# Kernel tuning notes

Measured on AMD Instinct MI355X. Metric: run time of the kernel, lower is better.

The kernel has to match this reference:

```python
import jax, jax.numpy as jnp
import numpy as np
from jax import lax

B, S, F, H, C = 256, 14, 1024, 1024, 2513


def setup_inputs() -> dict:
    key = jax.random.key(0)
    ks = jax.random.split(key, 12)
    s = 1.0 / np.sqrt(H)  # PyTorch LSTM/Linear init range
    u = lambda k, shape: jax.random.uniform(k, shape, jnp.float32, -s, s)
    return {
        "inputs": jax.random.normal(ks[0], (B, S, F), jnp.float32),
        # rolling LSTM params (PyTorch gate order: i, f, g, o)
        "Wih_r": u(ks[1], (4 * H, F)), "Whh_r": u(ks[2], (4 * H, H)),
        "bih_r": u(ks[3], (4 * H,)), "bhh_r": u(ks[4], (4 * H,)),
        # unrolling LSTM params
        "Wih_u": u(ks[5], (4 * H, F)), "Whh_u": u(ks[6], (4 * H, H)),
        "bih_u": u(ks[7], (4 * H,)), "bhh_u": u(ks[8], (4 * H,)),
        # classifier
        "Wc": u(ks[9], (C, H)), "bc": u(ks[10], (C,)),
    }


def _gate_update(gates, c):
    i, f, g, o = jnp.split(gates, 4, axis=-1)
    c2 = jax.nn.sigmoid(f) * c + jax.nn.sigmoid(i) * jnp.tanh(g)
    h2 = jax.nn.sigmoid(o) * jnp.tanh(c2)
    return h2, c2


def reference(inputs, Wih_r, Whh_r, bih_r, bhh_r, Wih_u, Whh_u, bih_u, bhh_u, Wc, bc):
    # dropout layers are identity (eval mode)
    x = inputs.transpose(1, 0, 2)  # [S, B, F]

    # --- rolling LSTM: collect h, c at every timestep ---
    xg_r = jnp.einsum('sbf,gf->sbg', x, Wih_r) + bih_r + bhh_r  # [S,B,4H]

    def roll_step(carry, xg_t):
        h, c = carry
        h2, c2 = _gate_update(xg_t + h @ Whh_r.T, c)
        return (h2, c2), (h2, c2)

    z = jnp.zeros((B, H), inputs.dtype)
    _, (hs, cs) = lax.scan(roll_step, (z, z), xg_r)  # [S,B,H] each

    # --- unrolling LSTM: for each t, feed inputs[t] repeated (S - t + 1) times,
    # starting from (hs[t], cs[t]); keep the final hidden state.
    # Vectorized: run S+1 steps for every t, gather step index S-t.
    xg_u = jnp.einsum('sbf,gf->sbg', x, Wih_u) + bih_u + bhh_u  # [S,B,4H] (input constant per t)

    def unroll_one(xg_t, h0, c0):
        def step(carry, _):
            h, c = carry
            h2, c2 = _gate_update(xg_t + h @ Whh_u.T, c)
            return (h2, c2), h2
        _, hs_all = lax.scan(step, (h0, c0), None, length=S + 1)
        return hs_all  # [S+1, B, H]

    allh = jax.vmap(unroll_one)(xg_u, hs, cs)  # [S, S+1, B, H]
    t_idx = jnp.arange(S)
    h_n = allh[t_idx, S - t_idx]  # last hidden of each length-(S-t+1) unroll -> [S,B,H]

    preds = h_n.transpose(1, 0, 2)  # [B, S, H]
    y = preds @ Wc.T + bc  # [B, S, C]
    return y
```

## Files before the change

### kernel.cpp

```cpp
#include <hip/hip_runtime.h>
#include <hip/hip_bf16.h>

#define GLOBAL_AS __attribute__((address_space(1)))
#define LDS_AS    __attribute__((address_space(3)))

typedef __bf16 bf16_t;
typedef __bf16 bf16x8 __attribute__((ext_vector_type(8)));
typedef __bf16 bf16x4 __attribute__((ext_vector_type(4)));
typedef float  f32x4  __attribute__((ext_vector_type(4)));
typedef _Float16 fp16_t;

static constexpr int Bb = 256;
static constexpr int Ss = 14;
static constexpr int Hh = 1024;
static constexpr int Cc = 2513;
static constexpr int NXc = 3584;
static constexpr int Kk = 1024;

__device__ __forceinline__ float sigm(float x)   { return 1.0f / (1.0f + __expf(-x)); }
__device__ __forceinline__ float tanh_f(float x) { return 2.0f / (1.0f + __expf(-2.0f * x)) - 1.0f; }

template<int EPI>
__global__ __launch_bounds__(256, 2)
void gemm_bt(const bf16_t* __restrict__ A, const bf16_t* __restrict__ Bm,
             int N, int rpg, int cpg, int CG, int CB,
             const float* __restrict__ e_bias,
             bf16_t* __restrict__ xg_bf,
             float* __restrict__ fout)
{
    const int lin = blockIdx.x;
    const int xcd = lin & 7;
    const int per = lin >> 3;
    const int rg = xcd / CG, cg = xcd % CG;
    const int rb = rg * rpg + per % rpg;
    const int cb = cg * cpg + per / rpg;
    if (cb >= CB) return;

    __shared__ char smem[32768];
    LDS_AS char* sA = (LDS_AS char*)smem;
    LDS_AS char* sB = sA + 16384;

    const int tid  = threadIdx.x;
    const int lane = tid & 63;
    const int wave = tid >> 6;
    const int row0 = rb * 128;
    const int col0 = cb * 128;
    const int mwb  = (wave >> 1) * 64;
    const int nwb  = (wave & 1) * 64;
    const int quad = lane >> 4;
    const int l15  = lane & 15;

    f32x4 acc[4][4] = {};

    for (int kb = 0; kb < Kk; kb += 64) {
#pragma unroll
        for (int it = 0; it < 4; ++it) {
            int c  = it * 256 + tid;
            int m  = c >> 3;
            int kq = (c & 7) ^ (m & 7);
            size_t arow;
            if (EPI == 2) {
                int row = row0 + m;
                int bb = row / 14;
                int ss = row - bb * 14;
                arow = (size_t)(ss * 256 + bb);
            } else {
                arow = (size_t)(row0 + m);
            }
            const bf16_t* ga = A + arow * Kk + kb + kq * 8;
            int nr = col0 + m;
            if (EPI == 2) { if (nr >= N) nr = 0; }
            const bf16_t* gb = Bm + (size_t)nr * Kk + kb + kq * 8;
            LDS_AS char* la = sA + (size_t)(it * 256 + (tid & 192)) * 16;
            LDS_AS char* lb = sB + (size_t)(it * 256 + (tid & 192)) * 16;
            __builtin_amdgcn_global_load_lds((const GLOBAL_AS void*)ga, (LDS_AS void*)la, 16, 0, 0);
            __builtin_amdgcn_global_load_lds((const GLOBAL_AS void*)gb, (LDS_AS void*)lb, 16, 0, 0);
        }
        __syncthreads();

#pragma unroll
        for (int kt = 0; kt < 2; ++kt) {
            bf16x8 af[4], bfr[4];
            const int kq = kt * 4 + quad;
#pragma unroll
            for (int i = 0; i < 4; ++i) {
                int ml = mwb + i * 16 + l15;
                af[i]  = *(const LDS_AS bf16x8*)(sA + (size_t)(ml * 8 + (kq ^ (ml & 7))) * 16);
                int nl = nwb + i * 16 + l15;
                bfr[i] = *(const LDS_AS bf16x8*)(sB + (size_t)(nl * 8 + (kq ^ (nl & 7))) * 16);
            }
#pragma unroll
            for (int i = 0; i < 4; ++i)
#pragma unroll
                for (int j = 0; j < 4; ++j)
                    acc[i][j] = __builtin_amdgcn_mfma_f32_16x16x32_bf16(af[i], bfr[j], acc[i][j], 0, 0, 0);
        }
        __syncthreads();
    }

#pragma unroll
    for (int im = 0; im < 4; ++im) {
#pragma unroll
        for (int jn = 0; jn < 4; ++jn) {
            const int rr  = row0 + mwb + im * 16 + quad * 4;
            const int col = col0 + nwb + jn * 16 + l15;
            f32x4 v = acc[im][jn];
            if (EPI == 0) {
                const int n = rr >> 2;
                f32x4 bi = *(const f32x4*)(e_bias + n * 4);
                bf16x4 o;
                o[0] = (bf16_t)(v[0] + bi[0]); o[1] = (bf16_t)(v[1] + bi[1]);
                o[2] = (bf16_t)(v[2] + bi[2]); o[3] = (bf16_t)(v[3] + bi[3]);
                *(bf16x4*)(xg_bf + ((size_t)n * NXc + col) * 4) = o;
            } else {
                if (col < N) {
                    float bi = e_bias[col];
#pragma unroll
                    for (int g = 0; g < 4; ++g)
                        fout[(size_t)(rr + g) * N + col] = v[g] + bi;
                }
            }
        }
    }
}

struct StepArgs {
    const bf16_t* Au;
    const bf16_t* Ar;
    const bf16_t* Bh;
    const bf16_t* xg_u;
    const bf16_t* xg_r;
    const fp16_t* c_r;
    fp16_t*       c_w;
    bf16_t*       h_w;
    int UCB;
    int b_off;
    int xg_off;
    int cr_off;
    int cw_off;
    int CB, cpg;
};

__global__ __launch_bounds__(256, 2)
void lstm_step(StepArgs p)
{
    const int lin = blockIdx.x;
    const int xcd = lin & 7;
    const int per = lin >> 3;
    const int rb = (xcd >> 2) * 16 + (per & 15);
    const int cb = (xcd & 3) * p.cpg + (per >> 4);
    if (cb >= p.CB) return;

    const bool roll = (cb >= p.UCB);
    const int  colb = roll ? (cb - p.UCB) : cb;
    const bf16_t* A = roll ? p.Ar : p.Au;
    const int bcol0 = colb * 128 + (roll ? p.b_off : 0);

    __shared__ char smem[32768];
    LDS_AS char* sA = (LDS_AS char*)smem;
    LDS_AS char* sB = sA + 16384;

    const int tid  = threadIdx.x;
    const int lane = tid & 63;
    const int wave = tid >> 6;
    const int row0 = rb * 128;
    const int mwb  = (wave >> 1) * 64;
    const int nwb  = (wave & 1) * 64;
    const int quad = lane >> 4;
    const int l15  = lane & 15;

    f32x4 acc[4][4] = {};

    for (int kb = 0; kb < Kk; kb += 64) {
#pragma unroll
        for (int it = 0; it < 4; ++it) {
            int c  = it * 256 + tid;
            int m  = c >> 3;
            int kq = (c & 7) ^ (m & 7);
            const bf16_t* ga = A    + (size_t)(row0  + m) * Kk + kb + kq * 8;
            const bf16_t* gb = p.Bh + (size_t)(bcol0 + m) * Kk + kb + kq * 8;
            LDS_AS char* la = sA + (size_t)(it * 256 + (tid & 192)) * 16;
            LDS_AS char* lb = sB + (size_t)(it * 256 + (tid & 192)) * 16;
            __builtin_amdgcn_global_load_lds((const GLOBAL_AS void*)ga, (LDS_AS void*)la, 16, 0, 0);
            __builtin_amdgcn_global_load_lds((const GLOBAL_AS void*)gb, (LDS_AS void*)lb, 16, 0, 0);
        }
        __syncthreads();

#pragma unroll
        for (int kt = 0; kt < 2; ++kt) {
            bf16x8 af[4], bfr[4];
            const int kq = kt * 4 + quad;
#pragma unroll
            for (int i = 0; i < 4; ++i) {
                int ml = mwb + i * 16 + l15;
                af[i]  = *(const LDS_AS bf16x8*)(sA + (size_t)(ml * 8 + (kq ^ (ml & 7))) * 16);
                int nl = nwb + i * 16 + l15;
                bfr[i] = *(const LDS_AS bf16x8*)(sB + (size_t)(nl * 8 + (kq ^ (nl & 7))) * 16);
            }
#pragma unroll
            for (int i = 0; i < 4; ++i)
#pragma unroll
                for (int j = 0; j < 4; ++j)
                    acc[i][j] = __builtin_amdgcn_mfma_f32_16x16x32_bf16(af[i], bfr[j], acc[i][j], 0, 0, 0);
        }
        __syncthreads();
    }

    const bf16_t* xg = roll ? p.xg_r : p.xg_u;
    const int xo = roll ? p.xg_off : 0;
    const int cro = roll ? p.cr_off : 0;
    const int cwo = roll ? p.cw_off : 0;

#pragma unroll
    for (int im = 0; im < 4; ++im) {
#pragma unroll
        for (int jn = 0; jn < 4; ++jn) {
            const int rr  = row0 + mwb + im * 16 + quad * 4;
            const int col = colb * 128 + nwb + jn * 16 + l15;
            f32x4 v = acc[im][jn];
            const int n = rr >> 2;
            bf16x4 xg4 = *(const bf16x4*)(xg + ((size_t)n * NXc + (col + xo)) * 4);
            float gi = v[0] + (float)xg4[0];
            float gf = v[1] + (float)xg4[1];
            float gg = v[2] + (float)xg4[2];
            float go = v[3] + (float)xg4[3];
            const size_t sr = (size_t)(col + cro) * Hh + n;
            const size_t sw = (size_t)(col + cwo) * Hh + n;
            float c2 = sigm(gf) * (float)p.c_r[sr] + sigm(gi) * tanh_f(gg);
            float h2 = sigm(go) * tanh_f(c2);
            p.c_w[sw] = (fp16_t)c2;
            p.h_w[sw] = (bf16_t)h2;
        }
    }
}

__global__ void cvt_w(const float* __restrict__ a0, const float* __restrict__ a1,
                      const float* __restrict__ a2, const float* __restrict__ a3,
                      bf16_t* __restrict__ o0, bf16_t* __restrict__ o1,
                      bf16_t* __restrict__ o2, bf16_t* __restrict__ o3)
{
    int idx = blockIdx.x * 256 + threadIdx.x;
    int mat = idx >> 20;
    int r   = (idx >> 8) & 4095;
    int k4  = (idx & 255) * 4;
    int n = r >> 2, g = r & 3;
    const float* src = mat == 0 ? a0 : mat == 1 ? a1 : mat == 2 ? a2 : a3;
    bf16_t*      dst = mat == 0 ? o0 : mat == 1 ? o1 : mat == 2 ? o2 : o3;
    f32x4 v = *(const f32x4*)(src + (size_t)(g * Hh + n) * Kk + k4);
    bf16x4 o;
    o[0] = (bf16_t)v[0]; o[1] = (bf16_t)v[1]; o[2] = (bf16_t)v[2]; o[3] = (bf16_t)v[3];
    *(bf16x4*)(dst + (size_t)r * Kk + k4) = o;
}

__global__ void cvt_bias(const float* __restrict__ bih_r, const float* __restrict__ bhh_r,
                         const float* __restrict__ bih_u, const float* __restrict__ bhh_u,
                         float* __restrict__ br, float* __restrict__ bu)
{
    int r = blockIdx.x * 256 + threadIdx.x;
    int n = r >> 2, g = r & 3;
    int ir = g * Hh + n;
    br[r] = bih_r[ir] + bhh_r[ir];
    bu[r] = bih_u[ir] + bhh_u[ir];
}

__global__ void cvt_x(const float* __restrict__ src, bf16_t* __restrict__ dst)
{
    int idx = blockIdx.x * 256 + threadIdx.x;
    int f4  = (idx & 255) * 4;
    int row = idx >> 8;
    int s = row % 14, b = row / 14;
    f32x4 v = *(const f32x4*)(src + (size_t)row * Kk + f4);
    bf16x4 o;
    o[0] = (bf16_t)v[0]; o[1] = (bf16_t)v[1]; o[2] = (bf16_t)v[2]; o[3] = (bf16_t)v[3];
    *(bf16x4*)(dst + (size_t)(s * 256 + b) * Kk + f4) = o;
}

__global__ void cast_f32_bf16(const float* __restrict__ src, bf16_t* __restrict__ dst, int n4)
{
    int i = blockIdx.x * 256 + threadIdx.x;
    if (i < n4) {
        f32x4 v = *(const f32x4*)(src + (size_t)i * 4);
        bf16x4 o;
        o[0] = (bf16_t)v[0]; o[1] = (bf16_t)v[1]; o[2] = (bf16_t)v[2]; o[3] = (bf16_t)v[3];
        *(bf16x4*)(dst + (size_t)i * 4) = o;
    }
}

extern "C" void kernel_launch(void* const* d_in, const int* in_sizes, int n_in,
                              void* d_out, int out_size, void* d_ws, size_t ws_size,
                              hipStream_t stream)
{
    const float* x_in  = (const float*)d_in[0];
    const float* Wih_r = (const float*)d_in[1];
    const float* Whh_r = (const float*)d_in[2];
    const float* bih_r = (const float*)d_in[3];
    const float* bhh_r = (const float*)d_in[4];
    const float* Wih_u = (const float*)d_in[5];
    const float* Whh_u = (const float*)d_in[6];
    const float* bih_u = (const float*)d_in[7];
    const float* bhh_u = (const float*)d_in[8];
    const float* Wc    = (const float*)d_in[9];
    const float* bc    = (const float*)d_in[10];
    float* out = (float*)d_out;

    char* ws = (char*)d_ws;
    size_t off = 0;
    auto alloc = [&](size_t bytes) -> char* {
        char* p = ws + off;
        off += (bytes + 255) & ~(size_t)255;
        return p;
    };

    const size_t BH = (size_t)Bb * Hh;
    bf16_t* w_ih2  = (bf16_t*)alloc((size_t)8192 * Kk * 2);
    bf16_t* w_hhr  = (bf16_t*)alloc((size_t)4096 * Kk * 2);
    bf16_t* w_hhu  = (bf16_t*)alloc((size_t)4096 * Kk * 2);
    bf16_t* wc_b   = (bf16_t*)alloc((size_t)Cc * Kk * 2);
    bf16_t* x_b    = (bf16_t*)alloc((size_t)NXc * Kk * 2);
    float*  bias2  = (float*)alloc(8192 * 4);
    bf16_t* XG2    = (bf16_t*)alloc((size_t)2048 * NXc * 4 * 2);
    bf16_t* P0     = (bf16_t*)alloc((size_t)Ss * BH * 2);
    bf16_t* P1     = (bf16_t*)alloc((size_t)Ss * BH * 2);
    fp16_t* Cp0    = (fp16_t*)alloc((size_t)Ss * BH * 2);
    fp16_t* Cp1    = (fp16_t*)alloc((size_t)Ss * BH * 2);
    bf16_t* h0     = (bf16_t*)alloc(BH * 2);
    fp16_t* c0     = (fp16_t*)alloc(BH * 2);

    bf16_t* XGr = XG2;
    bf16_t* XGu = XG2 + (size_t)1024 * NXc * 4;
    bf16_t* P[2] = {P0, P1};
    fp16_t* Cp[2] = {Cp0, Cp1};

    hipMemsetAsync(h0, 0, BH * 2, stream);
    hipMemsetAsync(c0, 0, BH * 2, stream);

    cvt_w<<<16384, 256, 0, stream>>>(Wih_r, Whh_r, Wih_u, Whh_u,
                                     w_ih2, w_hhr, w_ih2 + (size_t)4096 * Kk, w_hhu);
    cvt_bias<<<16, 256, 0, stream>>>(bih_r, bhh_r, bih_u, bhh_u, bias2, bias2 + 4096);
    cvt_x<<<3584, 256, 0, stream>>>(x_in, x_b);
    cast_f32_bf16<<<(Cc * Kk / 4 + 255) / 256, 256, 0, stream>>>(Wc, wc_b, Cc * Kk / 4);

    gemm_bt<0><<<1792, 256, 0, stream>>>(w_ih2, x_b, NXc, 16, 14, 2, 28,
                                         bias2, XG2, nullptr);

    for (int k = 1; k <= 16; ++k) {
        int a = (k - 1 < 14) ? (k - 1) : 14;
        int rollk = (k <= 14) ? 1 : 0;
        StepArgs p;
        p.Au = w_hhu;  p.Ar = w_hhr;
        p.Bh = (k == 1) ? h0 : P[(k - 1) & 1];
        p.xg_u = XGu;  p.xg_r = XGr;
        p.c_r = (k == 1) ? c0 : Cp[(k - 1) & 1];
        p.c_w = Cp[k & 1];
        p.h_w = P[k & 1];
        p.UCB = 2 * a;
        p.b_off  = (k >= 2) ? (k - 2) * 256 : 0;
        p.xg_off = (k - 1) * 256;
        p.cr_off = (k >= 2) ? (k - 2) * 256 : 0;
        p.cw_off = (k - 1) * 256;
        p.CB  = p.UCB + 2 * rollk;
        p.cpg = (p.CB + 3) >> 2;
        lstm_step<<<8 * 16 * p.cpg, 256, 0, stream>>>(p);
    }

    gemm_bt<2><<<560, 256, 0, stream>>>(P[0], wc_b, Cc, 14, 5, 4, 20,
                                        bc, nullptr, out);
}
```

Baseline: 872.1 us.

## Fuse LSTM step launches and classifier into one persistent kernel with counters

Replaces the 16 per-step LSTM kernel launches and the separate classifier GEMM with a single persistent kernel of 512 blocks. Blocks synchronise through per-column-block atomic counters, so a tile only waits for the tiles it depends on from the previous step instead of a full grid barrier. The hidden-state buffers are relaid out into a per-step history buffer. This removes launch overhead and lets steps overlap, at the cost of spin-wait polling and a co-residency assumption that could deadlock if the 512 blocks are not all resident.

```diff
diff --git a/kernel.cpp b/kernel.cpp
--- a/kernel.cpp
+++ b/kernel.cpp
@@ -9,6 +9,7 @@
 typedef __bf16 bf16x4 __attribute__((ext_vector_type(4)));
 typedef float  f32x4  __attribute__((ext_vector_type(4)));
 typedef _Float16 fp16_t;
+typedef _Float16 f16x2v __attribute__((ext_vector_type(2)));
 
 static constexpr int Bb = 256;
 static constexpr int Ss = 14;
@@ -20,13 +21,17 @@
 __device__ __forceinline__ float sigm(float x)   { return 1.0f / (1.0f + __expf(-x)); }
 __device__ __forceinline__ float tanh_f(float x) { return 2.0f / (1.0f + __expf(-2.0f * x)) - 1.0f; }
 
-template<int EPI>
+__device__ __forceinline__ int hoff(int k) {
+    if (k <= 0) return 0;
+    if (k <= 14) return 2 + k * (k - 1);
+    return (k == 15) ? 212 : 240;
+}
+
 __global__ __launch_bounds__(256, 2)
-void gemm_bt(const bf16_t* __restrict__ A, const bf16_t* __restrict__ Bm,
-             int N, int rpg, int cpg, int CG, int CB,
+void gemm_xg(const bf16_t* __restrict__ A, const bf16_t* __restrict__ Bm,
+             int rpg, int cpg, int CG, int CB,
              const float* __restrict__ e_bias,
-             bf16_t* __restrict__ xg_bf,
-             float* __restrict__ fout)
+             bf16_t* __restrict__ xg_bf)
 {
     const int lin = blockIdx.x;
     const int xcd = lin & 7;
@@ -58,26 +63,14 @@
             int c  = it * 256 + tid;
             int m  = c >> 3;
             int kq = (c & 7) ^ (m & 7);
-            size_t arow;
-            if (EPI == 2) {
-                int row = row0 + m;
-                int bb = row / 14;
-                int ss = row - bb * 14;
-                arow = (size_t)(ss * 256 + bb);
-            } else {
-                arow = (size_t)(row0 + m);
-            }
-            const bf16_t* ga = A + arow * Kk + kb + kq * 8;
-            int nr = col0 + m;
-            if (EPI == 2) { if (nr >= N) nr = 0; }
-            const bf16_t* gb = Bm + (size_t)nr * Kk + kb + kq * 8;
+            const bf16_t* ga = A + (size_t)(row0 + m) * Kk + kb + kq * 8;
+            const bf16_t* gb = Bm + (size_t)(col0 + m) * Kk + kb + kq * 8;
             LDS_AS char* la = sA + (size_t)(it * 256 + (tid & 192)) * 16;
             LDS_AS char* lb = sB + (size_t)(it * 256 + (tid & 192)) * 16;
             __builtin_amdgcn_global_load_lds((const GLOBAL_AS void*)ga, (LDS_AS void*)la, 16, 0, 0);
             __builtin_amdgcn_global_load_lds((const GLOBAL_AS void*)gb, (LDS_AS void*)lb, 16, 0, 0);
         }
         __syncthreads();
-
 #pragma unroll
         for (int kt = 0; kt < 2; ++kt) {
             bf16x8 af[4], bfr[4];
@@ -105,57 +98,33 @@
             const int rr  = row0 + mwb + im * 16 + quad * 4;
             const int col = col0 + nwb + jn * 16 + l15;
             f32x4 v = acc[im][jn];
-            if (EPI == 0) {
-                const int n = rr >> 2;
-                f32x4 bi = *(const f32x4*)(e_bias + n * 4);
-                bf16x4 o;
-                o[0] = (bf16_t)(v[0] + bi[0]); o[1] = (bf16_t)(v[1] + bi[1]);
-                o[2] = (bf16_t)(v[2] + bi[2]); o[3] = (bf16_t)(v[3] + bi[3]);
-                *(bf16x4*)(xg_bf + ((size_t)n * NXc + col) * 4) = o;
-            } else {
-                if (col < N) {
-                    float bi = e_bias[col];
-#pragma unroll
-                    for (int g = 0; g < 4; ++g)
-                        fout[(size_t)(rr + g) * N + col] = v[g] + bi;
-                }
-            }
+            const int n = rr >> 2;
+            f32x4 bi = *(const f32x4*)(e_bias + n * 4);
+            bf16x4 o;
+            o[0] = (bf16_t)(v[0] + bi[0]); o[1] = (bf16_t)(v[1] + bi[1]);
+            o[2] = (bf16_t)(v[2] + bi[2]); o[3] = (bf16_t)(v[3] + bi[3]);
+            *(bf16x4*)(xg_bf + ((size_t)n * NXc + col) * 4) = o;
         }
     }
 }
 
-struct StepArgs {
-    const bf16_t* Au;
-    const bf16_t* Ar;
-    const bf16_t* Bh;
+struct PArgs {
+    const bf16_t* w_hhu;
+    const bf16_t* w_hhr;
     const bf16_t* xg_u;
     const bf16_t* xg_r;
-    const fp16_t* c_r;
-    fp16_t*       c_w;
-    bf16_t*       h_w;
-    int UCB;
-    int b_off;
-    int xg_off;
-    int cr_off;
-    int cw_off;
-    int CB, cpg;
+    const bf16_t* wc;
+    bf16_t*  hbuf;
+    fp16_t*  c0;
+    fp16_t*  c1;
+    unsigned* cnt;
+    const float* bc;
+    float* out;
 };
 
 __global__ __launch_bounds__(256, 2)
-void lstm_step(StepArgs p)
-{
-    const int lin = blockIdx.x;
-    const int xcd = lin & 7;
-    const int per = lin >> 3;
-    const int rb = (xcd >> 2) * 16 + (per & 15);
-    const int cb = (xcd & 3) * p.cpg + (per >> 4);
-    if (cb >= p.CB) return;
-
-    const bool roll = (cb >= p.UCB);
-    const int  colb = roll ? (cb - p.UCB) : cb;
-    const bf16_t* A = roll ? p.Ar : p.Au;
-    const int bcol0 = colb * 128 + (roll ? p.b_off : 0);
-
+void lstm_persist(PArgs p)
+{
     __shared__ char smem[32768];
     LDS_AS char* sA = (LDS_AS char*)smem;
     LDS_AS char* sB = sA + 16384;
@@ -163,73 +132,185 @@
     const int tid  = threadIdx.x;
     const int lane = tid & 63;
     const int wave = tid >> 6;
-    const int row0 = rb * 128;
     const int mwb  = (wave >> 1) * 64;
     const int nwb  = (wave & 1) * 64;
     const int quad = lane >> 4;
     const int l15  = lane & 15;
-
-    f32x4 acc[4][4] = {};
-
-    for (int kb = 0; kb < Kk; kb += 64) {
-#pragma unroll
-        for (int it = 0; it < 4; ++it) {
-            int c  = it * 256 + tid;
-            int m  = c >> 3;
-            int kq = (c & 7) ^ (m & 7);
-            const bf16_t* ga = A    + (size_t)(row0  + m) * Kk + kb + kq * 8;
-            const bf16_t* gb = p.Bh + (size_t)(bcol0 + m) * Kk + kb + kq * 8;
-            LDS_AS char* la = sA + (size_t)(it * 256 + (tid & 192)) * 16;
-            LDS_AS char* lb = sB + (size_t)(it * 256 + (tid & 192)) * 16;
-            __builtin_amdgcn_global_load_lds((const GLOBAL_AS void*)ga, (LDS_AS void*)la, 16, 0, 0);
-            __builtin_amdgcn_global_load_lds((const GLOBAL_AS void*)gb, (LDS_AS void*)lb, 16, 0, 0);
-        }
-        __syncthreads();
-
-#pragma unroll
-        for (int kt = 0; kt < 2; ++kt) {
-            bf16x8 af[4], bfr[4];
-            const int kq = kt * 4 + quad;
-#pragma unroll
-            for (int i = 0; i < 4; ++i) {
-                int ml = mwb + i * 16 + l15;
-                af[i]  = *(const LDS_AS bf16x8*)(sA + (size_t)(ml * 8 + (kq ^ (ml & 7))) * 16);
-                int nl = nwb + i * 16 + l15;
-                bfr[i] = *(const LDS_AS bf16x8*)(sB + (size_t)(nl * 8 + (kq ^ (nl & 7))) * 16);
-            }
-#pragma unroll
-            for (int i = 0; i < 4; ++i)
-#pragma unroll
-                for (int j = 0; j < 4; ++j)
-                    acc[i][j] = __builtin_amdgcn_mfma_f32_16x16x32_bf16(af[i], bfr[j], acc[i][j], 0, 0, 0);
-        }
-        __syncthreads();
+    const int x    = blockIdx.x & 7;
+    const int lb   = blockIdx.x >> 3;
+    const int rbg  = x >> 2;
+    const int cmod = x & 3;
+
+    for (int k = 1; k <= 16; ++k) {
+        const int a   = (k - 1 < 14) ? (k - 1) : 14;
+        const int U2  = 2 * a;
+        const int ncu = (U2 > cmod) ? (((U2 - 1 - cmod) >> 2) + 1) : 0;
+        int rollC = -1;
+        if (k <= 14) {
+            int r0 = 2 * k - 2;
+            if ((r0 & 3) == cmod) rollC = r0;
+            else if (((r0 + 1) & 3) == cmod) rollC = r0 + 1;
+        }
+        const int nc = ncu + (rollC >= 0 ? 1 : 0);
+        const int T  = nc * 16;
+
+        for (int j = lb; j < T; j += 64) {
+            const int  ci   = j >> 4;
+            const int  rb   = rbg * 16 + (j & 15);
+            const bool roll = (ci >= ncu);
+            const int  cb   = roll ? rollC : (cmod + 4 * ci);
+
+            if (k > 1) {
+                const int dep = (k - 2) * 28 + (roll ? (cb - 2) : cb);
+                if (tid == 0)
+                    while (__hip_atomic_load(&p.cnt[dep], __ATOMIC_RELAXED,
+                                             __HIP_MEMORY_SCOPE_AGENT) < 32u)
+                        __builtin_amdgcn_s_sleep(1);
+            }
+            __syncthreads();
+
+            const bf16_t* A = (roll ? p.w_hhr : p.w_hhu) + (size_t)rb * (128 * Kk);
+            int bcb = roll ? (cb - 2) : cb; if (bcb < 0) bcb = 0;
+            const bf16_t* Bm = p.hbuf + ((size_t)(hoff(k - 1) + bcb) << 17);
+
+            f32x4 acc[4][4] = {};
+            for (int kb = 0; kb < Kk; kb += 64) {
+#pragma unroll
+                for (int it = 0; it < 4; ++it) {
+                    int c  = it * 256 + tid;
+                    int m  = c >> 3;
+                    int kq = (c & 7) ^ (m & 7);
+                    const bf16_t* ga = A  + (size_t)m * Kk + kb + kq * 8;
+                    const bf16_t* gb = Bm + (size_t)m * Kk + kb + kq * 8;
+                    LDS_AS char* la  = sA + (size_t)(it * 256 + (tid & 192)) * 16;
+                    LDS_AS char* lb2 = sB + (size_t)(it * 256 + (tid & 192)) * 16;
+                    __builtin_amdgcn_global_load_lds((const GLOBAL_AS void*)ga, (LDS_AS void*)la, 16, 0, 0);
+                    __builtin_amdgcn_global_load_lds((const GLOBAL_AS void*)gb, (LDS_AS void*)lb2, 16, 0, 0);
+                }
+                __syncthreads();
+#pragma unroll
+                for (int kt = 0; kt < 2; ++kt) {
+                    bf16x8 af[4], bfr[4];
+                    const int kq = kt * 4 + quad;
+#pragma unroll
+                    for (int i = 0; i < 4; ++i) {
+                        int ml = mwb + i * 16 + l15;
+                        af[i]  = *(const LDS_AS bf16x8*)(sA + (size_t)(ml * 8 + (kq ^ (ml & 7))) * 16);
+                        int nl = nwb + i * 16 + l15;
+                        bfr[i] = *(const LDS_AS bf16x8*)(sB + (size_t)(nl * 8 + (kq ^ (nl & 7))) * 16);
+                    }
+#pragma unroll
+                    for (int i2 = 0; i2 < 4; ++i2)
+#pragma unroll
+                        for (int j2 = 0; j2 < 4; ++j2)
+                            acc[i2][j2] = __builtin_amdgcn_mfma_f32_16x16x32_bf16(af[i2], bfr[j2], acc[i2][j2], 0, 0, 0);
+                }
+                __syncthreads();
+            }
+
+            const bf16_t* xg = roll ? p.xg_r : p.xg_u;
+            fp16_t*       cw = (k & 1) ? p.c1 : p.c0;
+            const fp16_t* cr = (k & 1) ? p.c0 : p.c1;
+            if (k == 1) cr = (const fp16_t*)p.hbuf;
+            const int crcol0 = bcb * 128;
+            const int cwcol0 = cb * 128;
+            bf16_t* hw = p.hbuf + ((size_t)(hoff(k) + cb) << 17);
+            const int row0 = rb * 128;
+#pragma unroll
+            for (int im = 0; im < 4; ++im) {
+#pragma unroll
+                for (int jn = 0; jn < 4; ++jn) {
+                    const int rr = row0 + mwb + im * 16 + quad * 4;
+                    const int cl = nwb + jn * 16 + l15;
+                    f32x4 v = acc[im][jn];
+                    const int n = rr >> 2;
+                    bf16x4 xg4 = *(const bf16x4*)(xg + ((size_t)n * NXc + (cb * 128 + cl)) * 4);
+                    float gi = v[0] + (float)xg4[0];
+                    float gf = v[1] + (float)xg4[1];
+                    float gg = v[2] + (float)xg4[2];
+                    float go = v[3] + (float)xg4[3];
+                    const unsigned* cp = (const unsigned*)(cr + ((size_t)(crcol0 + cl) << 10) + (n & ~1));
+                    unsigned cvb = __hip_atomic_load(cp, __ATOMIC_RELAXED, __HIP_MEMORY_SCOPE_AGENT);
+                    f16x2v cc; __builtin_memcpy(&cc, &cvb, 4);
+                    float cold = (float)cc[n & 1];
+                    float c2 = sigm(gf) * cold + sigm(gi) * tanh_f(gg);
+                    float h2 = sigm(go) * tanh_f(c2);
+                    cw[((size_t)(cwcol0 + cl) << 10) + n] = (fp16_t)c2;
+                    hw[((size_t)cl << 10) + n] = (bf16_t)h2;
+                }
+            }
+            __syncthreads();
+            if (tid == 0)
+                __hip_atomic_fetch_add(&p.cnt[(k - 1) * 28 + cb], 1u,
+                                       __ATOMIC_RELEASE, __HIP_MEMORY_SCOPE_AGENT);
+        }
     }
 
-    const bf16_t* xg = roll ? p.xg_r : p.xg_u;
-    const int xo = roll ? p.xg_off : 0;
-    const int cro = roll ? p.cr_off : 0;
-    const int cwo = roll ? p.cw_off : 0;
-
-#pragma unroll
-    for (int im = 0; im < 4; ++im) {
-#pragma unroll
-        for (int jn = 0; jn < 4; ++jn) {
-            const int rr  = row0 + mwb + im * 16 + quad * 4;
-            const int col = colb * 128 + nwb + jn * 16 + l15;
-            f32x4 v = acc[im][jn];
-            const int n = rr >> 2;
-            bf16x4 xg4 = *(const bf16x4*)(xg + ((size_t)n * NXc + (col + xo)) * 4);
-            float gi = v[0] + (float)xg4[0];
-            float gf = v[1] + (float)xg4[1];
-            float gg = v[2] + (float)xg4[2];
-            float go = v[3] + (float)xg4[3];
-            const size_t sr = (size_t)(col + cro) * Hh + n;
-            const size_t sw = (size_t)(col + cwo) * Hh + n;
-            float c2 = sigm(gf) * (float)p.c_r[sr] + sigm(gi) * tanh_f(gg);
-            float h2 = sigm(go) * tanh_f(c2);
-            p.c_w[sw] = (fp16_t)c2;
-            p.h_w[sw] = (bf16_t)h2;
+    if (tid == 0)
+        for (int c = 0; c < 28; ++c)
+            while (__hip_atomic_load(&p.cnt[15 * 28 + c], __ATOMIC_RELAXED,
+                                     __HIP_MEMORY_SCOPE_AGENT) < 32u)
+                __builtin_amdgcn_s_sleep(1);
+    __syncthreads();
+
+    const bf16_t* hf = p.hbuf + ((size_t)hoff(16) << 17);
+    for (int i = blockIdx.x; i < 560; i += 512) {
+        const int rb = i / 20, cbn = i % 20;
+        const int row0 = rb * 128, col0 = cbn * 128;
+
+        f32x4 acc[4][4] = {};
+        for (int kb = 0; kb < Kk; kb += 64) {
+#pragma unroll
+            for (int it = 0; it < 4; ++it) {
+                int c  = it * 256 + tid;
+                int m  = c >> 3;
+                int kq = (c & 7) ^ (m & 7);
+                int row = row0 + m;
+                int bb = row / 14;
+                int ss = row - bb * 14;
+                const bf16_t* ga = hf + (size_t)(ss * 256 + bb) * Kk + kb + kq * 8;
+                int nr = col0 + m; if (nr >= Cc) nr = 0;
+                const bf16_t* gb = p.wc + (size_t)nr * Kk + kb + kq * 8;
+                LDS_AS char* la  = sA + (size_t)(it * 256 + (tid & 192)) * 16;
+                LDS_AS char* lb2 = sB + (size_t)(it * 256 + (tid & 192)) * 16;
+                __builtin_amdgcn_global_load_lds((const GLOBAL_AS void*)ga, (LDS_AS void*)la, 16, 0, 0);
+                __builtin_amdgcn_global_load_lds((const GLOBAL_AS void*)gb, (LDS_AS void*)lb2, 16, 0, 0);
+            }
+            __syncthreads();
+#pragma unroll
+            for (int kt = 0; kt < 2; ++kt) {
+                bf16x8 af[4], bfr[4];
+                const int kq = kt * 4 + quad;
+#pragma unroll
+                for (int i2 = 0; i2 < 4; ++i2) {
+                    int ml = mwb + i2 * 16 + l15;
+                    af[i2]  = *(const LDS_AS bf16x8*)(sA + (size_t)(ml * 8 + (kq ^ (ml & 7))) * 16);
+                    int nl = nwb + i2 * 16 + l15;
+                    bfr[i2] = *(const LDS_AS bf16x8*)(sB + (size_t)(nl * 8 + (kq ^ (nl & 7))) * 16);
+                }
+#pragma unroll
+                for (int i2 = 0; i2 < 4; ++i2)
+#pragma unroll
+                    for (int j2 = 0; j2 < 4; ++j2)
+                        acc[i2][j2] = __builtin_amdgcn_mfma_f32_16x16x32_bf16(af[i2], bfr[j2], acc[i2][j2], 0, 0, 0);
+            }
+            __syncthreads();
+        }
+
+#pragma unroll
+        for (int im = 0; im < 4; ++im) {
+#pragma unroll
+            for (int jn = 0; jn < 4; ++jn) {
+                const int rr  = row0 + mwb + im * 16 + quad * 4;
+                const int col = col0 + nwb + jn * 16 + l15;
+                f32x4 v = acc[im][jn];
+                if (col < Cc) {
+                    float bi = p.bc[col];
+#pragma unroll
+                    for (int g = 0; g < 4; ++g)
+                        p.out[(size_t)(rr + g) * Cc + col] = v[g] + bi;
+                }
+            }
         }
     }
 }
@@ -311,28 +392,20 @@
         return p;
     };
 
-    const size_t BH = (size_t)Bb * Hh;
-    bf16_t* w_ih2  = (bf16_t*)alloc((size_t)8192 * Kk * 2);
-    bf16_t* w_hhr  = (bf16_t*)alloc((size_t)4096 * Kk * 2);
-    bf16_t* w_hhu  = (bf16_t*)alloc((size_t)4096 * Kk * 2);
-    bf16_t* wc_b   = (bf16_t*)alloc((size_t)Cc * Kk * 2);
-    bf16_t* x_b    = (bf16_t*)alloc((size_t)NXc * Kk * 2);
-    float*  bias2  = (float*)alloc(8192 * 4);
-    bf16_t* XG2    = (bf16_t*)alloc((size_t)2048 * NXc * 4 * 2);
-    bf16_t* P0     = (bf16_t*)alloc((size_t)Ss * BH * 2);
-    bf16_t* P1     = (bf16_t*)alloc((size_t)Ss * BH * 2);
-    fp16_t* Cp0    = (fp16_t*)alloc((size_t)Ss * BH * 2);
-    fp16_t* Cp1    = (fp16_t*)alloc((size_t)Ss * BH * 2);
-    bf16_t* h0     = (bf16_t*)alloc(BH * 2);
-    fp16_t* c0     = (fp16_t*)alloc(BH * 2);
-
-    bf16_t* XGr = XG2;
-    bf16_t* XGu = XG2 + (size_t)1024 * NXc * 4;
-    bf16_t* P[2] = {P0, P1};
-    fp16_t* Cp[2] = {Cp0, Cp1};
-
-    hipMemsetAsync(h0, 0, BH * 2, stream);
-    hipMemsetAsync(c0, 0, BH * 2, stream);
+    bf16_t*   w_ih2 = (bf16_t*)alloc((size_t)8192 * Kk * 2);
+    bf16_t*   w_hhr = (bf16_t*)alloc((size_t)4096 * Kk * 2);
+    bf16_t*   w_hhu = (bf16_t*)alloc((size_t)4096 * Kk * 2);
+    bf16_t*   wc_b  = (bf16_t*)alloc((size_t)Cc * Kk * 2);
+    bf16_t*   x_b   = (bf16_t*)alloc((size_t)NXc * Kk * 2);
+    float*    bias2 = (float*)alloc(8192 * 4);
+    bf16_t*   XG2   = (bf16_t*)alloc((size_t)2048 * NXc * 4 * 2);
+    bf16_t*   hbuf  = (bf16_t*)alloc((size_t)268 * 131072 * 2);
+    fp16_t*   c0b   = (fp16_t*)alloc((size_t)NXc * Kk * 2);
+    fp16_t*   c1b   = (fp16_t*)alloc((size_t)NXc * Kk * 2);
+    unsigned* cnt   = (unsigned*)alloc(16 * 28 * 4);
+
+    hipMemsetAsync(hbuf, 0, (size_t)2 * 131072 * 2, stream);
+    hipMemsetAsync(cnt, 0, 16 * 28 * 4, stream);
 
     cvt_w<<<16384, 256, 0, stream>>>(Wih_r, Whh_r, Wih_u, Whh_u,
                                      w_ih2, w_hhr, w_ih2 + (size_t)4096 * Kk, w_hhu);
@@ -340,29 +413,19 @@
     cvt_x<<<3584, 256, 0, stream>>>(x_in, x_b);
     cast_f32_bf16<<<(Cc * Kk / 4 + 255) / 256, 256, 0, stream>>>(Wc, wc_b, Cc * Kk / 4);
 
-    gemm_bt<0><<<1792, 256, 0, stream>>>(w_ih2, x_b, NXc, 16, 14, 2, 28,
-                                         bias2, XG2, nullptr);
-
-    for (int k = 1; k <= 16; ++k) {
-        int a = (k - 1 < 14) ? (k - 1) : 14;
-        int rollk = (k <= 14) ? 1 : 0;
-        StepArgs p;
-        p.Au = w_hhu;  p.Ar = w_hhr;
-        p.Bh = (k == 1) ? h0 : P[(k - 1) & 1];
-        p.xg_u = XGu;  p.xg_r = XGr;
-        p.c_r = (k == 1) ? c0 : Cp[(k - 1) & 1];
-        p.c_w = Cp[k & 1];
-        p.h_w = P[k & 1];
-        p.UCB = 2 * a;
-        p.b_off  = (k >= 2) ? (k - 2) * 256 : 0;
-        p.xg_off = (k - 1) * 256;
-        p.cr_off = (k >= 2) ? (k - 2) * 256 : 0;
-        p.cw_off = (k - 1) * 256;
-        p.CB  = p.UCB + 2 * rollk;
-        p.cpg = (p.CB + 3) >> 2;
-        lstm_step<<<8 * 16 * p.cpg, 256, 0, stream>>>(p);
-    }
-
-    gemm_bt<2><<<560, 256, 0, stream>>>(P[0], wc_b, Cc, 14, 5, 4, 20,
-                                        bc, nullptr, out);
-}
+    gemm_xg<<<1792, 256, 0, stream>>>(w_ih2, x_b, 16, 14, 2, 28, bias2, XG2);
+
+    PArgs p;
+    p.w_hhu = w_hhu;
+    p.w_hhr = w_hhr;
+    p.xg_u  = XG2 + (size_t)1024 * NXc * 4;
+    p.xg_r  = XG2;
+    p.wc    = wc_b;
+    p.hbuf  = hbuf;
+    p.c0    = c0b;
+    p.c1    = c1b;
+    p.cnt   = cnt;
+    p.bc    = bc;
+    p.out   = out;
+    lstm_persist<<<512, 256, 0, stream>>>(p);
+}
```

After: 1.442 ms. +65.3%, slower.
